# Kernel optimization log

Hardware: AMD Instinct MI355X
Metric: run time of the kernel (lower is better)

## Reference

```python
import jax, jax.numpy as jnp
import numpy as np

B, N, C = 4, 2048, 1024
H = 16
D = C // H  # head_dim = 64
NEG = -1e9


def setup_inputs() -> dict:
    key = jax.random.key(0)
    k1, k2, k3, k4 = jax.random.split(key, 4)
    x = jax.random.normal(k1, (B, N, C), dtype=jnp.float32)
    # additive causal mask [N, N]: 0 on/below diagonal, -1e9 above
    causal = jnp.tril(jnp.ones((N, N), dtype=bool))
    attn_mask = jnp.where(causal, 0.0, NEG).astype(jnp.float32)
    # params: qkv Dense (no bias, qkv_bias=False), proj Dense (with bias)
    W_qkv = jax.random.normal(k2, (C, 3 * C), dtype=jnp.float32) / np.sqrt(C)
    W_proj = jax.random.normal(k3, (C, C), dtype=jnp.float32) / np.sqrt(C)
    b_proj = jnp.zeros((C,), dtype=jnp.float32)
    return {"x": x, "attn_mask": attn_mask, "W_qkv": W_qkv,
            "W_proj": W_proj, "b_proj": b_proj}


def reference(x, attn_mask, W_qkv, W_proj, b_proj):
    b, n, c = x.shape
    # qkv projection -> [B, N, 3, H, D] -> q,k,v each [B, H, N, D]
    qkv = (x @ W_qkv).reshape(b, n, 3, H, D)
    qkv = jnp.transpose(qkv, (2, 0, 3, 1, 4))
    q, k, v = qkv[0], qkv[1], qkv[2]
    # unfused attention: full [B, H, N, N] score matrix
    scores = jnp.einsum('bhnd,bhmd->bhnm', q, k) / np.sqrt(D).astype(jnp.float32)
    scores = scores + attn_mask  # broadcast [N, N] over batch/heads
    attn_w = jax.nn.softmax(scores.astype(jnp.float32), axis=-1).astype(scores.dtype)
    out = jnp.einsum('bhnm,bhmd->bhnd', attn_w, v)
    out = jnp.transpose(out, (0, 2, 1, 3)).reshape(b, n, c)
    return out @ W_proj + b_proj
```

## Files before the change

### kernel.cpp

```cpp
#include <hip/hip_runtime.h>
#include <stdint.h>


typedef short s16x8 __attribute__((ext_vector_type(8)));
typedef short s16x4 __attribute__((ext_vector_type(4)));
typedef float f32x4 __attribute__((ext_vector_type(4)));
typedef unsigned int u32;

__device__ __forceinline__ uint16_t f2bf(float f) {
  union { float f; uint32_t u; } v; v.f = f;
  uint32_t r = v.u + 0x7fffu + ((v.u >> 16) & 1u);
  return (uint16_t)(r >> 16);
}

__device__ __forceinline__ u32 cvt_pk_bf16(float lo, float hi) {
  u32 r;
  asm("v_cvt_pk_bf16_f32 %0, %1, %2" : "=v"(r) : "v"(lo), "v"(hi));
  return r;
}

__device__ __forceinline__ s16x8 pack4(u32 w0, u32 w1, u32 w2, u32 w3) {
  union { u32 u[4]; s16x8 v; } t;
  t.u[0] = w0; t.u[1] = w1; t.u[2] = w2; t.u[3] = w3;
  return t.v;
}

__device__ __forceinline__ s16x8 pack2h(s16x4 a, s16x4 b) {
  union { s16x4 h[2]; s16x8 v; } t;
  t.h[0] = a; t.h[1] = b;
  return t.v;
}

#define GLOAD_LDS16(g, l)                                            \
  __builtin_amdgcn_global_load_lds(                                  \
      (const __attribute__((address_space(1))) void*)(g),            \
      (__attribute__((address_space(3))) void*)(l), 16, 0, 0)

__device__ __forceinline__ void transpose32_body(
    const float* __restrict__ src, uint16_t* __restrict__ dst,
    int R, int C, int bx32, int by32, uint16_t (*tile)[33], int tid) {
  const int tx = tid & 31, ty = tid >> 5;
#pragma unroll
  for (int i = 0; i < 32; i += 8)
    tile[ty + i][tx] = f2bf(src[(size_t)(by32 + ty + i) * C + bx32 + tx]);
  __syncthreads();
#pragma unroll
  for (int i = 0; i < 32; i += 8)
    dst[(size_t)(bx32 + ty + i) * R + by32 + tx] = tile[tx][ty + i];
}

__global__ __launch_bounds__(256) void prep_kernel(
    const float* __restrict__ x, uint16_t* __restrict__ xbf,
    const float* __restrict__ Wqkv, uint16_t* __restrict__ wqkvT,
    const float* __restrict__ Wproj, uint16_t* __restrict__ wprojT) {
  __shared__ uint16_t tile[32][33];
  const int bid = blockIdx.x;
  if (bid < 4096) {
    const int i = bid * 256 + threadIdx.x;
    const f32x4 a = ((const f32x4*)x)[2 * i];
    const f32x4 b = ((const f32x4*)x)[2 * i + 1];
    s16x8 r;
    r[0] = (short)f2bf(a[0]); r[1] = (short)f2bf(a[1]);
    r[2] = (short)f2bf(a[2]); r[3] = (short)f2bf(a[3]);
    r[4] = (short)f2bf(b[0]); r[5] = (short)f2bf(b[1]);
    r[6] = (short)f2bf(b[2]); r[7] = (short)f2bf(b[3]);
    ((s16x8*)xbf)[i] = r;
  } else if (bid < 4096 + 3072) {
    const int t = bid - 4096;
    transpose32_body(Wqkv, wqkvT, 1024, 3072, (t % 96) * 32, (t / 96) * 32,
                     tile, threadIdx.x);
  } else {
    const int t = bid - 7168;
    transpose32_body(Wproj, wprojT, 1024, 1024, (t & 31) * 32, (t >> 5) * 32,
                     tile, threadIdx.x);
  }
}

__global__ __launch_bounds__(256) void vtrans_kernel(
    const uint16_t* __restrict__ src, uint16_t* __restrict__ dst) {
  const int bh = blockIdx.y >> 1, dhalf = blockIdx.y & 1;
  const int n0 = blockIdx.x * 32, d0 = dhalf * 32;
  const uint16_t* sb = src + (size_t)bh * 131072;
  uint16_t* db = dst + (size_t)bh * 131072;
  __shared__ uint16_t tile[32][33];
  const int tx = threadIdx.x & 31, ty = threadIdx.x >> 5;
#pragma unroll
  for (int i = 0; i < 32; i += 8)
    tile[ty + i][tx] = sb[(size_t)(n0 + ty + i) * 64 + d0 + tx];
  __syncthreads();
#pragma unroll
  for (int i = 0; i < 32; i += 8)
    db[(size_t)(d0 + ty + i) * 2048 + n0 + tx] = tile[tx][ty + i];
}

template <bool ROUTE>
__global__ __launch_bounds__(256) void gemm_bt_kernel(
    const uint16_t* __restrict__ A, const uint16_t* __restrict__ Bt,
    float* __restrict__ Cout,
    uint16_t* __restrict__ rq, uint16_t* __restrict__ rk, uint16_t* __restrict__ rv,
    const float* __restrict__ bias, int M, int N, int K) {
  __shared__ uint16_t sA[128 * 64];
  __shared__ uint16_t sB[128 * 64];
  const int tid = threadIdx.x;
  const int lane = tid & 63, w = tid >> 6;
  const int l15 = lane & 15, quad = lane >> 4;
  const int row0 = blockIdx.y * 128, col0 = blockIdx.x * 128;
  const int wm = (w >> 1) * 64, wn = (w & 1) * 64;

  f32x4 acc[4][4];
#pragma unroll
  for (int i = 0; i < 4; ++i)
#pragma unroll
    for (int j = 0; j < 4; ++j)
#pragma unroll
      for (int e = 0; e < 4; ++e) acc[i][j][e] = 0.0f;

  const int sx = l15 & 7;
  const int ok[2] = {((0 * 4 + quad) ^ sx) * 8, ((1 * 4 + quad) ^ sx) * 8};

  for (int k0 = 0; k0 < K; k0 += 64) {
    __syncthreads();
#pragma unroll
    for (int i = 0; i < 4; ++i) {
      const int cbase = i * 256 + w * 64;
      const int c = cbase + lane;
      const int r = c >> 3;
      const int kc = ((c & 7) ^ (r & 7)) * 8;
      GLOAD_LDS16(A + (size_t)(row0 + r) * K + k0 + kc, sA + cbase * 8);
      GLOAD_LDS16(Bt + (size_t)(col0 + r) * K + k0 + kc, sB + cbase * 8);
    }
    __syncthreads();

#pragma unroll
    for (int kk = 0; kk < 2; ++kk) {
      s16x8 aF[4], bF[4];
#pragma unroll
      for (int mt = 0; mt < 4; ++mt)
        aF[mt] = *(const s16x8*)(sA + (wm + mt * 16 + l15) * 64 + ok[kk]);
#pragma unroll
      for (int nt = 0; nt < 4; ++nt)
        bF[nt] = *(const s16x8*)(sB + (wn + nt * 16 + l15) * 64 + ok[kk]);
#pragma unroll
      for (int mt = 0; mt < 4; ++mt)
#pragma unroll
        for (int nt = 0; nt < 4; ++nt)
          acc[mt][nt] = __builtin_amdgcn_mfma_f32_16x16x32_bf16(aF[mt], bF[nt], acc[mt][nt], 0, 0, 0);
    }
  }

  if (ROUTE) {
    const int which = col0 >> 10;
    uint16_t* dst = (which == 0) ? rq : ((which == 1) ? rk : rv);
    const float qs = (which == 0) ? 0.18033688011112042f : 1.0f;
#pragma unroll
    for (int mt = 0; mt < 4; ++mt) {
#pragma unroll
      for (int nt = 0; nt < 4; ++nt) {
        const int colg0 = col0 + wn + nt * 16;
        const int h = (colg0 >> 6) & 15, d0 = colg0 & 63;
#pragma unroll
        for (int i = 0; i < 4; ++i) {
          const int rowg = row0 + wm + mt * 16 + quad * 4 + i;
          const int bh = ((rowg >> 11) << 4) + h, n = rowg & 2047;
          dst[(size_t)bh * 131072 + (size_t)n * 64 + d0 + l15] = f2bf(acc[mt][nt][i] * qs);
        }
      }
    }
  } else {
#pragma unroll
    for (int mt = 0; mt < 4; ++mt) {
#pragma unroll
      for (int nt = 0; nt < 4; ++nt) {
        const int colg = col0 + wn + nt * 16 + l15;
        const float bv = bias[colg];
#pragma unroll
        for (int i = 0; i < 4; ++i) {
          const int rowg = row0 + wm + mt * 16 + quad * 4 + i;
          Cout[(size_t)rowg * N + colg] = acc[mt][nt][i] + bv;
        }
      }
    }
  }
}

__global__ __launch_bounds__(256) void attn_kernel(
    const uint16_t* __restrict__ q_ws, const uint16_t* __restrict__ k_ws,
    const uint16_t* __restrict__ vt_ws, uint16_t* __restrict__ out) {
  const int p = blockIdx.x;
  const int bh = blockIdx.y;
  const int b = bh >> 4, h = bh & 15;
  const int q0L = p * 64, q0H = (31 - p) * 64;
  const int tid = threadIdx.x;
  const int lane = tid & 63, w = tid >> 6;
  const int l15 = lane & 15, quad = lane >> 4;

  const uint16_t* qb = q_ws + (size_t)bh * 131072;
  const uint16_t* kb = k_ws + (size_t)bh * 131072;
  const uint16_t* vtb = vt_ws + (size_t)bh * 131072;

  __shared__ uint16_t sK[2][64 * 64];
  __shared__ uint16_t sV[2][64 * 64];

  const int qrowL = q0L + w * 16 + l15;
  const int qrowH = q0H + w * 16 + l15;
  const s16x8 aQL0 = *(const s16x8*)(qb + (size_t)qrowL * 64 + quad * 8);
  const s16x8 aQL1 = *(const s16x8*)(qb + (size_t)qrowL * 64 + 32 + quad * 8);
  const s16x8 aQH0 = *(const s16x8*)(qb + (size_t)qrowH * 64 + quad * 8);
  const s16x8 aQH1 = *(const s16x8*)(qb + (size_t)qrowH * 64 + 32 + quad * 8);

  f32x4 oL[4], oH[4], laccL, laccH;
#pragma unroll
  for (int e = 0; e < 4; ++e) { laccL[e] = 0.0f; laccH[e] = 0.0f; }
#pragma unroll
  for (int i = 0; i < 4; ++i)
#pragma unroll
    for (int e = 0; e < 4; ++e) { oL[i][e] = 0.0f; oH[i][e] = 0.0f; }

  s16x8 bOnes;
#pragma unroll
  for (int j = 0; j < 8; ++j) bOnes[j] = (short)0x3F80;

  const int vr = tid >> 2, dc = (tid & 3) * 16;
  const int wc0 = ((tid & 3) * 2 + 0) ^ (vr & 7);
  const int wc1 = ((tid & 3) * 2 + 1) ^ (vr & 7);
  s16x8 rk0 = *(const s16x8*)(kb + (size_t)vr * 64 + dc);
  s16x8 rk1 = *(const s16x8*)(kb + (size_t)vr * 64 + dc + 8);
  s16x8 rv0 = *(const s16x8*)(vtb + (size_t)vr * 2048 + dc);
  s16x8 rv1 = *(const s16x8*)(vtb + (size_t)vr * 2048 + dc + 8);

  const int sx = l15 & 7;
  const int okK0 = (quad ^ sx) * 8;
  const int okK1 = ((quad + 4) ^ sx) * 8;
  const int ovA[2] = {((0 + (quad >> 1)) ^ sx) * 8 + (quad & 1) * 4,
                      ((4 + (quad >> 1)) ^ sx) * 8 + (quad & 1) * 4};
  const int ovB[2] = {((2 + (quad >> 1)) ^ sx) * 8 + (quad & 1) * 4,
                      ((6 + (quad >> 1)) ^ sx) * 8 + (quad & 1) * 4};

  const int qrel = w * 16 + l15;

  auto qkt = [&](const s16x8& a0, const s16x8& a1, const uint16_t* sKb,
                 f32x4 (&s)[4]) {
#pragma unroll
    for (int nt = 0; nt < 4; ++nt) {
      f32x4 z;
#pragma unroll
      for (int e = 0; e < 4; ++e) z[e] = 0.0f;
      const s16x8 bK0 = *(const s16x8*)(sKb + (nt * 16 + l15) * 64 + okK0);
      const s16x8 bK1 = *(const s16x8*)(sKb + (nt * 16 + l15) * 64 + okK1);
      s[nt] = __builtin_amdgcn_mfma_f32_16x16x32_bf16(bK0, a0, z, 0, 0, 0);
      s[nt] = __builtin_amdgcn_mfma_f32_16x16x32_bf16(bK1, a1, s[nt], 0, 0, 0);
    }
  };

  auto finish = [&](const f32x4 (&s)[4], bool diag, f32x4* o, f32x4& lacc,
                    const uint16_t* sVb) {
#pragma unroll
    for (int kk = 0; kk < 2; ++kk) {
      u32 wlo[2], whi[2];
#pragma unroll
      for (int t2 = 0; t2 < 2; ++t2) {
        const f32x4& sv = s[2 * kk + t2];
        float pp[4];
        if (diag) {
          const int nt = 2 * kk + t2;
#pragma unroll
          for (int i = 0; i < 4; ++i) {
            const int kv = nt * 16 + quad * 4 + i;
            pp[i] = (kv > qrel) ? 0.0f : __builtin_amdgcn_exp2f(sv[i]);
          }
        } else {
#pragma unroll
          for (int i = 0; i < 4; ++i) pp[i] = __builtin_amdgcn_exp2f(sv[i]);
        }
        wlo[t2] = cvt_pk_bf16(pp[0], pp[1]);
        whi[t2] = cvt_pk_bf16(pp[2], pp[3]);
      }
      const s16x8 aP = pack4(wlo[0], whi[0], wlo[1], whi[1]);
      lacc = __builtin_amdgcn_mfma_f32_16x16x32_bf16(aP, bOnes, lacc, 0, 0, 0);
#pragma unroll
      for (int dblk = 0; dblk < 4; ++dblk) {
        const uint16_t* vrow = sVb + (dblk * 16 + l15) * 64;
        const s16x4 b0 = *(const s16x4*)(vrow + ovA[kk]);
        const s16x4 b1 = *(const s16x4*)(vrow + ovB[kk]);
        const s16x8 bV = pack2h(b0, b1);
        o[dblk] = __builtin_amdgcn_mfma_f32_16x16x32_bf16(aP, bV, o[dblk], 0, 0, 0);
      }
    }
  };

  const int TH = q0H >> 6;
  const int TL = q0L >> 6;
  f32x4 sHp[4], sLp[4];

  for (int t = 0; t <= TH; ++t) {
    const int buf = t & 1;
    uint16_t* sKb = sK[buf];
    uint16_t* sVb = sV[buf];
    *(s16x8*)(sKb + vr * 64 + wc0 * 8) = rk0;
    *(s16x8*)(sKb + vr * 64 + wc1 * 8) = rk1;
    *(s16x8*)(sVb + vr * 64 + wc0 * 8) = rv0;
    *(s16x8*)(sVb + vr * 64 + wc1 * 8) = rv1;
    if (t < TH) {
      const int kvn = (t + 1) << 6;
      rk0 = *(const s16x8*)(kb + (size_t)(kvn + vr) * 64 + dc);
      rk1 = *(const s16x8*)(kb + (size_t)(kvn + vr) * 64 + dc + 8);
      rv0 = *(const s16x8*)(vtb + (size_t)vr * 2048 + kvn + dc);
      rv1 = *(const s16x8*)(vtb + (size_t)vr * 2048 + kvn + dc + 8);
    }
    if (t >= 1) {
      finish(sHp, false, oH, laccH, sV[buf ^ 1]);
      if (t - 1 <= TL) finish(sLp, (t - 1) == TL, oL, laccL, sV[buf ^ 1]);
    }
    __syncthreads();
    qkt(aQH0, aQH1, sKb, sHp);
    if (t <= TL) qkt(aQL0, aQL1, sKb, sLp);
  }
  finish(sHp, true, oH, laccH, sV[TH & 1]);

  const size_t obase = (size_t)b * 2048 * 1024 + (size_t)h * 64;
  auto epi = [&](f32x4* o, const f32x4& lacc, int q0) {
#pragma unroll
    for (int i = 0; i < 4; ++i) {
      const float invi = 1.0f / lacc[i];
      const int row = q0 + w * 16 + quad * 4 + i;
#pragma unroll
      for (int dblk = 0; dblk < 4; ++dblk)
        out[obase + (size_t)row * 1024 + dblk * 16 + l15] = f2bf(o[dblk][i] * invi);
    }
  };
  epi(oH, laccH, q0H);
  epi(oL, laccL, q0L);
}

extern "C" void kernel_launch(void* const* d_in, const int* in_sizes, int n_in,
                              void* d_out, int out_size, void* d_ws, size_t ws_size,
                              hipStream_t stream) {
  (void)in_sizes; (void)n_in; (void)out_size; (void)ws_size;
  const float* x     = (const float*)d_in[0];
  const float* Wqkv  = (const float*)d_in[2];
  const float* Wproj = (const float*)d_in[3];
  const float* bproj = (const float*)d_in[4];
  float* outp = (float*)d_out;

  uint16_t* ws      = (uint16_t*)d_ws;
  uint16_t* q_ws    = ws;
  uint16_t* k_ws    = ws + (size_t)8388608;
  uint16_t* v_ws    = ws + (size_t)16777216;
  uint16_t* attn_ws = ws + (size_t)16777216;
  uint16_t* wqkvT   = ws + (size_t)25165824;
  uint16_t* wprojT  = ws + (size_t)28311552;
  uint16_t* xbf     = (uint16_t*)d_out;
  uint16_t* vt_ws   = (uint16_t*)d_out;

  prep_kernel<<<8192, 256, 0, stream>>>(x, xbf, Wqkv, wqkvT, Wproj, wprojT);
  gemm_bt_kernel<true><<<dim3(24, 64), 256, 0, stream>>>(
      xbf, wqkvT, nullptr, q_ws, k_ws, v_ws, nullptr, 8192, 3072, 1024);
  vtrans_kernel<<<dim3(64, 128), 256, 0, stream>>>(v_ws, vt_ws);
  attn_kernel<<<dim3(16, 64), 256, 0, stream>>>(q_ws, k_ws, vt_ws, attn_ws);
  gemm_bt_kernel<false><<<dim3(8, 64), 256, 0, stream>>>(
      attn_ws, wprojT, outp, nullptr, nullptr, nullptr, bproj, 8192, 1024, 1024);
}
```

Before: 271.4 us.

## Fuse V transpose into QKV GEMM epilogue and store attention output head-major

Removes the separate V-transpose kernel by having the QKV GEMM blocks that produce V stage their tile through LDS and write V transposed directly. The attention kernel now writes its output in per-head [bh][n][d] layout, overwriting the Q buffer in place. The projection GEMM gathers A from that head-major layout through address arithmetic. This saves one launch and a round trip of V through memory. In exchange it adds an extra LDS pass in the GEMM epilogue and relies on each attention block reading its Q rows before overwriting them.

New measurement: 267.1 us. Within noise of the previous version (-1.6%).

```diff
diff --git a/kernel.cpp b/kernel.cpp
--- a/kernel.cpp
+++ b/kernel.cpp
@@ -5,6 +5,7 @@
 typedef short s16x8 __attribute__((ext_vector_type(8)));
 typedef short s16x4 __attribute__((ext_vector_type(4)));
 typedef float f32x4 __attribute__((ext_vector_type(4)));
+typedef int i32x2 __attribute__((ext_vector_type(2)));
 typedef unsigned int u32;
 
 __device__ __forceinline__ uint16_t f2bf(float f) {
@@ -76,29 +77,11 @@
   }
 }
 
-__global__ __launch_bounds__(256) void vtrans_kernel(
-    const uint16_t* __restrict__ src, uint16_t* __restrict__ dst) {
-  const int bh = blockIdx.y >> 1, dhalf = blockIdx.y & 1;
-  const int n0 = blockIdx.x * 32, d0 = dhalf * 32;
-  const uint16_t* sb = src + (size_t)bh * 131072;
-  uint16_t* db = dst + (size_t)bh * 131072;
-  __shared__ uint16_t tile[32][33];
-  const int tx = threadIdx.x & 31, ty = threadIdx.x >> 5;
-#pragma unroll
-  for (int i = 0; i < 32; i += 8)
-    tile[ty + i][tx] = sb[(size_t)(n0 + ty + i) * 64 + d0 + tx];
-  __syncthreads();
-#pragma unroll
-  for (int i = 0; i < 32; i += 8)
-    db[(size_t)(d0 + ty + i) * 2048 + n0 + tx] = tile[tx][ty + i];
-}
-
-template <bool ROUTE>
-__global__ __launch_bounds__(256) void gemm_bt_kernel(
+__global__ __launch_bounds__(256) void gemm1_kernel(
     const uint16_t* __restrict__ A, const uint16_t* __restrict__ Bt,
-    float* __restrict__ Cout,
-    uint16_t* __restrict__ rq, uint16_t* __restrict__ rk, uint16_t* __restrict__ rv,
-    const float* __restrict__ bias, int M, int N, int K) {
+    uint16_t* __restrict__ rq, uint16_t* __restrict__ rk,
+    uint16_t* __restrict__ vt) {
+  constexpr int K = 1024;
   __shared__ uint16_t sA[128 * 64];
   __shared__ uint16_t sB[128 * 64];
   const int tid = threadIdx.x;
@@ -148,9 +131,39 @@
     }
   }
 
-  if (ROUTE) {
-    const int which = col0 >> 10;
-    uint16_t* dst = (which == 0) ? rq : ((which == 1) ? rk : rv);
+  const int which = col0 >> 10;
+  if (which == 2) {
+    __syncthreads();
+    uint16_t* tw = (w < 2) ? (sA + w * 4096) : (sB + (w - 2) * 4096);
+    const int colg0 = col0 + wn;
+    const int h = (colg0 >> 6) & 15;
+    const int rbase = row0 + wm;
+    const int bq = rbase >> 11, n0 = rbase & 2047;
+    const int bh = bq * 16 + h;
+    const int coff = quad >> 1;
+    const int boff = (quad & 1) * 4;
+#pragma unroll
+    for (int mt = 0; mt < 4; ++mt) {
+#pragma unroll
+      for (int nt = 0; nt < 4; ++nt) {
+        const int dloc = nt * 16 + l15;
+        const int phys = (mt * 2 + coff) ^ (dloc & 7);
+        i32x2 pr;
+        pr[0] = (int)cvt_pk_bf16(acc[mt][nt][0], acc[mt][nt][1]);
+        pr[1] = (int)cvt_pk_bf16(acc[mt][nt][2], acc[mt][nt][3]);
+        *(i32x2*)(tw + dloc * 64 + phys * 8 + boff) = pr;
+      }
+    }
+    const int d = lane;
+    uint16_t* vg = vt + (size_t)bh * 131072 + (size_t)d * 2048 + n0;
+#pragma unroll
+    for (int j = 0; j < 8; ++j) {
+      const int phys = j ^ (d & 7);
+      const s16x8 r = *(const s16x8*)(tw + d * 64 + phys * 8);
+      *(s16x8*)(vg + j * 8) = r;
+    }
+  } else {
+    uint16_t* dst = (which == 0) ? rq : rk;
     const float qs = (which == 0) ? 0.18033688011112042f : 1.0f;
 #pragma unroll
     for (int mt = 0; mt < 4; ++mt) {
@@ -166,29 +179,85 @@
         }
       }
     }
-  } else {
-#pragma unroll
-    for (int mt = 0; mt < 4; ++mt) {
-#pragma unroll
-      for (int nt = 0; nt < 4; ++nt) {
-        const int colg = col0 + wn + nt * 16 + l15;
-        const float bv = bias[colg];
-#pragma unroll
-        for (int i = 0; i < 4; ++i) {
-          const int rowg = row0 + wm + mt * 16 + quad * 4 + i;
-          Cout[(size_t)rowg * N + colg] = acc[mt][nt][i] + bv;
-        }
+  }
+}
+
+__global__ __launch_bounds__(256) void gemm2_kernel(
+    const uint16_t* __restrict__ Aq, const uint16_t* __restrict__ Bt,
+    float* __restrict__ Cout, const float* __restrict__ bias) {
+  constexpr int N = 1024, K = 1024;
+  __shared__ uint16_t sA[128 * 64];
+  __shared__ uint16_t sB[128 * 64];
+  const int tid = threadIdx.x;
+  const int lane = tid & 63, w = tid >> 6;
+  const int l15 = lane & 15, quad = lane >> 4;
+  const int row0 = blockIdx.y * 128, col0 = blockIdx.x * 128;
+  const int wm = (w >> 1) * 64, wn = (w & 1) * 64;
+
+  f32x4 acc[4][4];
+#pragma unroll
+  for (int i = 0; i < 4; ++i)
+#pragma unroll
+    for (int j = 0; j < 4; ++j)
+#pragma unroll
+      for (int e = 0; e < 4; ++e) acc[i][j][e] = 0.0f;
+
+  const int sx = l15 & 7;
+  const int ok[2] = {((0 * 4 + quad) ^ sx) * 8, ((1 * 4 + quad) ^ sx) * 8};
+
+  for (int k0 = 0; k0 < K; k0 += 64) {
+    __syncthreads();
+#pragma unroll
+    for (int i = 0; i < 4; ++i) {
+      const int cbase = i * 256 + w * 64;
+      const int c = cbase + lane;
+      const int r = c >> 3;
+      const int kc = ((c & 7) ^ (r & 7)) * 8;
+      const int row = row0 + r, k = k0 + kc;
+      const size_t aoff = ((size_t)(row >> 11) << 21) + ((size_t)(k >> 6) << 17) +
+                          ((size_t)(row & 2047) << 6) + (size_t)(k & 63);
+      GLOAD_LDS16(Aq + aoff, sA + cbase * 8);
+      GLOAD_LDS16(Bt + (size_t)(col0 + r) * K + k0 + kc, sB + cbase * 8);
+    }
+    __syncthreads();
+
+#pragma unroll
+    for (int kk = 0; kk < 2; ++kk) {
+      s16x8 aF[4], bF[4];
+#pragma unroll
+      for (int mt = 0; mt < 4; ++mt)
+        aF[mt] = *(const s16x8*)(sA + (wm + mt * 16 + l15) * 64 + ok[kk]);
+#pragma unroll
+      for (int nt = 0; nt < 4; ++nt)
+        bF[nt] = *(const s16x8*)(sB + (wn + nt * 16 + l15) * 64 + ok[kk]);
+#pragma unroll
+      for (int mt = 0; mt < 4; ++mt)
+#pragma unroll
+        for (int nt = 0; nt < 4; ++nt)
+          acc[mt][nt] = __builtin_amdgcn_mfma_f32_16x16x32_bf16(aF[mt], bF[nt], acc[mt][nt], 0, 0, 0);
+    }
+  }
+
+#pragma unroll
+  for (int mt = 0; mt < 4; ++mt) {
+#pragma unroll
+    for (int nt = 0; nt < 4; ++nt) {
+      const int colg = col0 + wn + nt * 16 + l15;
+      const float bv = bias[colg];
+#pragma unroll
+      for (int i = 0; i < 4; ++i) {
+        const int rowg = row0 + wm + mt * 16 + quad * 4 + i;
+        Cout[(size_t)rowg * N + colg] = acc[mt][nt][i] + bv;
       }
     }
   }
 }
 
 __global__ __launch_bounds__(256) void attn_kernel(
-    const uint16_t* __restrict__ q_ws, const uint16_t* __restrict__ k_ws,
-    const uint16_t* __restrict__ vt_ws, uint16_t* __restrict__ out) {
+    const uint16_t* q_ws, const uint16_t* __restrict__ k_ws,
+    const uint16_t* __restrict__ vt_ws, uint16_t* outq) {
   const int p = blockIdx.x;
   const int bh = blockIdx.y;
-  const int b = bh >> 4, h = bh & 15;
   const int q0L = p * 64, q0H = (31 - p) * 64;
   const int tid = threadIdx.x;
   const int lane = tid & 63, w = tid >> 6;
@@ -317,7 +386,7 @@
   }
   finish(sHp, true, oH, laccH, sV[TH & 1]);
 
-  const size_t obase = (size_t)b * 2048 * 1024 + (size_t)h * 64;
+  uint16_t* ob = outq + (size_t)bh * 131072;
   auto epi = [&](f32x4* o, const f32x4& lacc, int q0) {
 #pragma unroll
     for (int i = 0; i < 4; ++i) {
@@ -325,7 +394,7 @@
       const int row = q0 + w * 16 + quad * 4 + i;
 #pragma unroll
       for (int dblk = 0; dblk < 4; ++dblk)
-        out[obase + (size_t)row * 1024 + dblk * 16 + l15] = f2bf(o[dblk][i] * invi);
+        ob[(size_t)row * 64 + dblk * 16 + l15] = f2bf(o[dblk][i] * invi);
     }
   };
   epi(oH, laccH, q0H);
@@ -345,18 +414,13 @@
   uint16_t* ws      = (uint16_t*)d_ws;
   uint16_t* q_ws    = ws;
   uint16_t* k_ws    = ws + (size_t)8388608;
-  uint16_t* v_ws    = ws + (size_t)16777216;
-  uint16_t* attn_ws = ws + (size_t)16777216;
+  uint16_t* vt_ws   = ws + (size_t)16777216;
   uint16_t* wqkvT   = ws + (size_t)25165824;
   uint16_t* wprojT  = ws + (size_t)28311552;
   uint16_t* xbf     = (uint16_t*)d_out;
-  uint16_t* vt_ws   = (uint16_t*)d_out;
 
   prep_kernel<<<8192, 256, 0, stream>>>(x, xbf, Wqkv, wqkvT, Wproj, wprojT);
-  gemm_bt_kernel<true><<<dim3(24, 64), 256, 0, stream>>>(
-      xbf, wqkvT, nullptr, q_ws, k_ws, v_ws, nullptr, 8192, 3072, 1024);
-  vtrans_kernel<<<dim3(64, 128), 256, 0, stream>>>(v_ws, vt_ws);
-  attn_kernel<<<dim3(16, 64), 256, 0, stream>>>(q_ws, k_ws, vt_ws, attn_ws);
-  gemm_bt_kernel<false><<<dim3(8, 64), 256, 0, stream>>>(
-      attn_ws, wprojT, outp, nullptr, nullptr, nullptr, bproj, 8192, 1024, 1024);
-}
+  gemm1_kernel<<<dim3(24, 64), 256, 0, stream>>>(xbf, wqkvT, q_ws, k_ws, vt_ws);
+  attn_kernel<<<dim3(16, 64), 256, 0, stream>>>(q_ws, k_ws, vt_ws, q_ws);
+  gemm2_kernel<<<dim3(8, 64), 256, 0, stream>>>(q_ws, wprojT, outp, bproj);
+}
```
